# Kernel tuning notes

Hardware: AMD Instinct MI355X
Metric: run time of the kernel (lower is better)

Reference implementation:

```python
import jax, jax.numpy as jnp
import numpy as np

MAX_SCALE_MUL = float(np.log(100.0))
EPS = 1e-12

def _l2norm(t):
    # F.normalize(dim=-1): x / max(||x||_2, eps)
    n = jnp.sqrt(jnp.sum(t * t, axis=-1, keepdims=True))
    return t / jnp.maximum(n, EPS)

def setup_inputs() -> dict:
    key = jax.random.key(0)
    ks = jax.random.split(key, 6)
    B, L, C, H = 2, 2048, 1024, 16
    x = jax.random.normal(ks[0], (B, L, C), dtype=jnp.float32)
    attn_bias = jax.random.normal(ks[1], (1, 1, L, L), dtype=jnp.float32) * 0.02
    W_qkv = jax.random.normal(ks[2], (3 * C, C), dtype=jnp.float32) * (1.0 / np.sqrt(C))
    q_bias = jnp.zeros((C,), dtype=jnp.float32)
    v_bias = jnp.zeros((C,), dtype=jnp.float32)
    scale_mul_1H11 = jnp.full((1, H, 1, 1), np.log(4.0), dtype=jnp.float32)
    W_proj = jax.random.normal(ks[3], (C, C), dtype=jnp.float32) * (1.0 / np.sqrt(C))
    b_proj = jnp.zeros((C,), dtype=jnp.float32)
    return {"x": x, "attn_bias": attn_bias, "W_qkv": W_qkv, "q_bias": q_bias,
            "v_bias": v_bias, "scale_mul_1H11": scale_mul_1H11,
            "W_proj": W_proj, "b_proj": b_proj}

def reference(x, attn_bias, W_qkv, q_bias, v_bias, scale_mul_1H11, W_proj, b_proj):
    B, L, C = x.shape
    H = scale_mul_1H11.shape[1]
    D = C // H
    # qkv projection (no linear bias) + concatenated (q_bias, 0, v_bias)
    bias = jnp.concatenate([q_bias, jnp.zeros_like(q_bias), v_bias])
    pre_qkv = jnp.einsum('blc,oc->blo', x, W_qkv) + bias  # (B,L,3C)
    qkv = pre_qkv.reshape(B, L, 3, H, D).transpose(2, 0, 3, 1, 4)  # (3,B,H,L,D)
    q, k, v = qkv[0], qkv[1], qkv[2]
    # cosine attention: l2-normalize q,k; q scaled by learned per-head scale
    scale_mul = jnp.exp(jnp.minimum(scale_mul_1H11, MAX_SCALE_MUL))
    q = _l2norm(q) * scale_mul
    k = _l2norm(k)
    # slow_attn_original with scale=1 (attn_l2_norm path)
    attn = jnp.einsum('bhld,bhmd->bhlm', q, k) + attn_bias  # (B,H,L,L)
    attn = jax.nn.softmax(attn, axis=-1)
    oup = jnp.einsum('bhlm,bhmd->bhld', attn, v)  # (B,H,L,D)
    oup = oup.transpose(0, 2, 1, 3).reshape(B, L, C)
    return jnp.einsum('blc,oc->blo', oup, W_proj) + b_proj
```

## Files before the change

### kernel.cpp

```cpp
#include <hip/hip_runtime.h>

typedef short bf16x8 __attribute__((ext_vector_type(8)));
typedef unsigned short u16x8 __attribute__((ext_vector_type(8)));
typedef float f32x4 __attribute__((ext_vector_type(4)));
typedef float f32x16 __attribute__((ext_vector_type(16)));
typedef unsigned int u32x2 __attribute__((ext_vector_type(2)));

#define LOG2E 1.44269504088896340736f

__device__ __forceinline__ float bf2f(unsigned short u) {
  union { unsigned int i; float f; } v; v.i = ((unsigned int)u) << 16; return v.f;
}
__device__ __forceinline__ unsigned short f2bf(float f) {
  union { float fl; unsigned int i; } v; v.fl = f;
  unsigned int r = v.i + 0x7FFFu + ((v.i >> 16) & 1u);
  return (unsigned short)(r >> 16);
}
__device__ __forceinline__ unsigned int cvt_pk_bf16(float lo, float hi) {
  unsigned int d;
  asm("v_cvt_pk_bf16_f32 %0, %1, %2" : "=v"(d) : "v"(lo), "v"(hi));
  return d;
}
__device__ __forceinline__ void perm_swap(unsigned int& a, unsigned int& b) {
  asm("v_permlane32_swap_b32 %0, %1" : "+v"(a), "+v"(b));
}
__device__ __forceinline__ bf16x8 mk8(unsigned int a, unsigned int b,
                                      unsigned int c, unsigned int d) {
  union { unsigned int u[4]; bf16x8 v; } r;
  r.u[0] = a; r.u[1] = b; r.u[2] = c; r.u[3] = d;
  return r.v;
}
__device__ __forceinline__ void gload_lds16(const void* g, void* l) {
  __builtin_amdgcn_global_load_lds(
      (const __attribute__((address_space(1))) void*)g,
      (__attribute__((address_space(3))) void*)l, 16, 0, 0);
}

__global__ __launch_bounds__(256) void cvt_all(const float* __restrict__ x,
                                               const float* __restrict__ wqkv,
                                               const float* __restrict__ wproj,
                                               unsigned short* __restrict__ xb,
                                               unsigned short* __restrict__ wqb,
                                               unsigned short* __restrict__ wpb) {
  int i = blockIdx.x * 256 + threadIdx.x;
  const float* src; unsigned short* dst; int off;
  if (i < 524288)       { src = x;     dst = xb;  off = i; }
  else if (i < 917504)  { src = wqkv;  dst = wqb; off = i - 524288; }
  else                  { src = wproj; dst = wpb; off = i - 917504; }
  float4 a = ((const float4*)src)[2 * off];
  float4 b = ((const float4*)src)[2 * off + 1];
  u16x8 o;
  o[0] = f2bf(a.x); o[1] = f2bf(a.y); o[2] = f2bf(a.z); o[3] = f2bf(a.w);
  o[4] = f2bf(b.x); o[5] = f2bf(b.y); o[6] = f2bf(b.z); o[7] = f2bf(b.w);
  ((u16x8*)dst)[off] = o;
}

__global__ __launch_bounds__(256) void prep_bias(const float* __restrict__ bias,
                                                 unsigned short* __restrict__ biasArr) {
  int tid = blockIdx.x * 256 + threadIdx.x;
  int kg = tid & 1;
  int l = (tid >> 1) & 63;
  int w = (tid >> 7) & 3;
  int kb = (tid >> 9) & 31;
  int qt = (tid >> 14) & 15;
  int q = qt * 128 + w * 32 + (l & 31);
  int kbase = kb * 64 + kg * 32 + (l >> 5) * 4;
  const float* src = bias + (size_t)q * 2048 + kbase;
  u16x8 oa, ob;
#pragma unroll
  for (int rr = 0; rr < 4; ++rr) {
    float4 g = *(const float4*)(src + rr * 8);
    unsigned short e0 = f2bf(g.x * LOG2E), e1 = f2bf(g.y * LOG2E);
    unsigned short e2 = f2bf(g.z * LOG2E), e3 = f2bf(g.w * LOG2E);
    if (rr < 2) {
      oa[rr * 4 + 0] = e0; oa[rr * 4 + 1] = e1; oa[rr * 4 + 2] = e2; oa[rr * 4 + 3] = e3;
    } else {
      ob[(rr - 2) * 4 + 0] = e0; ob[(rr - 2) * 4 + 1] = e1;
      ob[(rr - 2) * 4 + 2] = e2; ob[(rr - 2) * 4 + 3] = e3;
    }
  }
  int base = (((qt * 32 + kb) * 4 + w) * 4 + kg * 2) * 64 + l;
  ((u16x8*)biasArr)[base] = oa;
  ((u16x8*)biasArr)[base + 64] = ob;
}

template <bool F32OUT>
__global__ __launch_bounds__(256) void gemm_nt(const unsigned short* __restrict__ A,
                                               const unsigned short* __restrict__ B,
                                               void* __restrict__ Cout,
                                               const float* __restrict__ bias,
                                               int M, int N, int K) {
  __shared__ __align__(16) unsigned short a_lds[128 * 64];
  __shared__ __align__(16) unsigned short b_lds[128 * 64];
  const int t = threadIdx.x;
  const int lane = t & 63, w = t >> 6;
  const int wm = w >> 1, wn = w & 1;
  const int r16 = lane >> 4, c16 = lane & 15;
  const int m0 = blockIdx.y * 128, n0 = blockIdx.x * 128;
  f32x4 acc[4][4] = {};
  for (int k0 = 0; k0 < K; k0 += 64) {
#pragma unroll
    for (int i = 0; i < 4; ++i) {
      int s = i * 256 + t;
      int row = s >> 3, c = s & 7;
      int cs = c ^ (row & 7);
      gload_lds16(A + (size_t)(m0 + row) * K + k0 + cs * 8, (char*)a_lds + s * 16);
      gload_lds16(B + (size_t)(n0 + row) * K + k0 + cs * 8, (char*)b_lds + s * 16);
    }
    __syncthreads();
#pragma unroll
    for (int ks = 0; ks < 2; ++ks) {
      bf16x8 af[4], bfr[4];
#pragma unroll
      for (int mi = 0; mi < 4; ++mi) {
        int row = wm * 64 + mi * 16 + c16;
        int ch = (r16 + ks * 4) ^ (row & 7);
        af[mi] = *(const bf16x8*)&a_lds[row * 64 + ch * 8];
      }
#pragma unroll
      for (int ni = 0; ni < 4; ++ni) {
        int row = wn * 64 + ni * 16 + c16;
        int ch = (r16 + ks * 4) ^ (row & 7);
        bfr[ni] = *(const bf16x8*)&b_lds[row * 64 + ch * 8];
      }
#pragma unroll
      for (int mi = 0; mi < 4; ++mi)
#pragma unroll
        for (int ni = 0; ni < 4; ++ni)
          acc[mi][ni] = __builtin_amdgcn_mfma_f32_16x16x32_bf16(af[mi], bfr[ni], acc[mi][ni], 0, 0, 0);
    }
    __syncthreads();
  }
#pragma unroll
  for (int mi = 0; mi < 4; ++mi)
#pragma unroll
    for (int ni = 0; ni < 4; ++ni)
#pragma unroll
      for (int r = 0; r < 4; ++r) {
        int m = m0 + wm * 64 + mi * 16 + r16 * 4 + r;
        int n = n0 + wn * 64 + ni * 16 + c16;
        float v = acc[mi][ni][r];
        if constexpr (F32OUT) {
          ((float*)Cout)[(size_t)m * N + n] = v + bias[n];
        } else {
          ((unsigned short*)Cout)[(size_t)m * N + n] = f2bf(v);
        }
      }
}

__global__ __launch_bounds__(256) void norm_pack(const unsigned short* __restrict__ pre,
                                                 const float* __restrict__ q_bias,
                                                 const float* __restrict__ v_bias,
                                                 const float* __restrict__ scale_mul,
                                                 unsigned short* __restrict__ qo,
                                                 unsigned short* __restrict__ ko,
                                                 unsigned short* __restrict__ vto) {
  __shared__ float tl[64][65];
  const int t = threadIdx.x;
  const int li = t >> 2, dq = t & 3;
  const int tile = blockIdx.x;
  const int sl = blockIdx.y;
  const int qkv = sl >> 4, h = sl & 15;
  const int b = tile >> 5, lt = tile & 31;
  const int l = lt * 64 + li;
  const int dbase = dq * 16;
  const unsigned short* src = pre + ((size_t)b * 2048 + l) * 3072 + qkv * 1024 + h * 64 + dbase;
  float v[16];
  bf16x8 x0 = *(const bf16x8*)src;
  bf16x8 x1 = *(const bf16x8*)(src + 8);
#pragma unroll
  for (int j = 0; j < 8; ++j) {
    v[j] = bf2f((unsigned short)x0[j]);
    v[8 + j] = bf2f((unsigned short)x1[j]);
  }
  if (qkv == 0) {
#pragma unroll
    for (int j = 0; j < 16; ++j) v[j] += q_bias[h * 64 + dbase + j];
  } else if (qkv == 2) {
#pragma unroll
    for (int j = 0; j < 16; ++j) v[j] += v_bias[h * 64 + dbase + j];
  }
  if (qkv < 2) {
    float ss = 0.f;
#pragma unroll
    for (int j = 0; j < 16; ++j) ss += v[j] * v[j];
    ss += __shfl_xor(ss, 1);
    ss += __shfl_xor(ss, 2);
    float inv = 1.0f / fmaxf(sqrtf(ss), 1e-12f);
    if (qkv == 0) inv *= __expf(fminf(scale_mul[h], 4.6051701859880914f));
    u16x8 o0, o1;
#pragma unroll
    for (int j = 0; j < 8; ++j) {
      o0[j] = f2bf(v[j] * inv);
      o1[j] = f2bf(v[8 + j] * inv);
    }
    unsigned short* dst = (qkv == 0 ? qo : ko) + ((size_t)(b * 16 + h) * 2048 + l) * 64 + dbase;
    *(u16x8*)dst = o0;
    *(u16x8*)(dst + 8) = o1;
  } else {
#pragma unroll
    for (int j = 0; j < 16; ++j) tl[li][dbase + j] = v[j];
    __syncthreads();
    const int d = li;
    const int lb = dq * 16;
    u16x8 o0, o1;
#pragma unroll
    for (int j = 0; j < 8; ++j) {
      o0[j] = f2bf(tl[lb + j][d]);
      o1[j] = f2bf(tl[lb + 8 + j][d]);
    }
    unsigned short* dst = vto + ((size_t)(b * 16 + h) * 64 + d) * 2048 + lt * 64 + lb;
    *(u16x8*)dst = o0;
    *(u16x8*)(dst + 8) = o1;
  }
}

__global__ __launch_bounds__(256) void attn_fwd(const unsigned short* __restrict__ qb,
                                                const unsigned short* __restrict__ kbuf,
                                                const unsigned short* __restrict__ vtb,
                                                const unsigned short* __restrict__ biasArr,
                                                unsigned short* __restrict__ oup) {
  __shared__ __align__(16) unsigned short k_lds[4096];
  __shared__ __align__(16) unsigned short vt_lds[4096];
  __shared__ __align__(16) unsigned short b_lds[8192];
  const int t = threadIdx.x;
  const int lane = t & 63, w = t >> 6;
  const int l31 = lane & 31, hi = lane >> 5;
  const int bid = blockIdx.x;
  const int swz = (bid & 7) * 64 + (bid >> 3);
  const int bh = swz >> 4;
  const int qt = swz & 15;
  const int q0 = qt * 128;
  const int h = bh & 15;
  const size_t base = (size_t)bh * 2048 * 64;
  const unsigned short* kp = kbuf + base + (size_t)(t & 31) * 64 +
                             ((t >> 6) & 3) * 16 + ((t >> 5) & 1) * 8;
  const unsigned short* vp = vtb + base + (size_t)(t & 31) * 2048 +
                             ((t >> 6) & 3) * 16 + ((t >> 5) & 1) * 8;
  const unsigned short* bsrc = biasArr + (size_t)qt * 262144 + t * 8;
  bf16x8 qf[4];
  {
    const unsigned short* qp = qb + base + (size_t)(q0 + w * 32 + l31) * 64 + hi * 8;
    qf[0] = *(const bf16x8*)qp;
    qf[1] = *(const bf16x8*)(qp + 16);
    qf[2] = *(const bf16x8*)(qp + 32);
    qf[3] = *(const bf16x8*)(qp + 48);
  }
  f32x16 o0 = {}, o1 = {};
  float ls0 = 0.f, ls1 = 0.f;
  const unsigned short* bl = b_lds + w * 2048 + lane * 8;

  for (int kb = 0; kb < 32; ++kb) {
    gload_lds16(kp + (size_t)kb * 4096, (char*)k_lds + t * 16);
    gload_lds16(kp + (size_t)kb * 4096 + 2048, (char*)k_lds + t * 16 + 4096);
    gload_lds16(vp + kb * 64, (char*)vt_lds + t * 16);
    gload_lds16(vp + kb * 64 + 32 * 2048, (char*)vt_lds + t * 16 + 4096);
#pragma unroll
    for (int i = 0; i < 4; ++i)
      gload_lds16(bsrc + kb * 8192 + i * 2048, (char*)b_lds + t * 16 + i * 4096);
    __syncthreads();
    f32x16 s0 = {}, s1 = {};
    __builtin_amdgcn_s_setprio(1);
#pragma unroll
    for (int dc = 0; dc < 4; ++dc) {
      bf16x8 kf0 = *(const bf16x8*)&k_lds[dc * 512 + lane * 8];
      bf16x8 kf1 = *(const bf16x8*)&k_lds[(4 + dc) * 512 + lane * 8];
      s0 = __builtin_amdgcn_mfma_f32_32x32x16_bf16(kf0, qf[dc], s0, 0, 0, 0);
      s1 = __builtin_amdgcn_mfma_f32_32x32x16_bf16(kf1, qf[dc], s1, 0, 0, 0);
    }
    __builtin_amdgcn_s_setprio(0);
    bf16x8 b0 = *(const bf16x8*)(bl);
    bf16x8 b1 = *(const bf16x8*)(bl + 512);
    bf16x8 b2 = *(const bf16x8*)(bl + 1024);
    bf16x8 b3 = *(const bf16x8*)(bl + 1536);
    float p0[16], p1[16];
#pragma unroll
    for (int r = 0; r < 8; ++r) {
      p0[r] = __builtin_amdgcn_exp2f(__builtin_fmaf(s0[r], LOG2E, bf2f((unsigned short)b0[r])));
      p0[8 + r] = __builtin_amdgcn_exp2f(__builtin_fmaf(s0[8 + r], LOG2E, bf2f((unsigned short)b1[r])));
      p1[r] = __builtin_amdgcn_exp2f(__builtin_fmaf(s1[r], LOG2E, bf2f((unsigned short)b2[r])));
      p1[8 + r] = __builtin_amdgcn_exp2f(__builtin_fmaf(s1[8 + r], LOG2E, bf2f((unsigned short)b3[r])));
    }
#pragma unroll
    for (int r = 0; r < 16; ++r) { ls0 += p0[r]; ls1 += p1[r]; }
    unsigned int x0 = cvt_pk_bf16(p0[0], p0[1]), x1 = cvt_pk_bf16(p0[2], p0[3]);
    unsigned int y0 = cvt_pk_bf16(p0[4], p0[5]), y1 = cvt_pk_bf16(p0[6], p0[7]);
    unsigned int z0 = cvt_pk_bf16(p0[8], p0[9]), z1 = cvt_pk_bf16(p0[10], p0[11]);
    unsigned int w0 = cvt_pk_bf16(p0[12], p0[13]), w1 = cvt_pk_bf16(p0[14], p0[15]);
    perm_swap(x0, y0); perm_swap(x1, y1); perm_swap(z0, w0); perm_swap(z1, w1);
    bf16x8 pf0 = mk8(x0, x1, y0, y1);
    bf16x8 pf1 = mk8(z0, z1, w0, w1);
    unsigned int a0 = cvt_pk_bf16(p1[0], p1[1]), a1 = cvt_pk_bf16(p1[2], p1[3]);
    unsigned int c0 = cvt_pk_bf16(p1[4], p1[5]), c1 = cvt_pk_bf16(p1[6], p1[7]);
    unsigned int d0 = cvt_pk_bf16(p1[8], p1[9]), d1 = cvt_pk_bf16(p1[10], p1[11]);
    unsigned int e0 = cvt_pk_bf16(p1[12], p1[13]), e1 = cvt_pk_bf16(p1[14], p1[15]);
    perm_swap(a0, c0); perm_swap(a1, c1); perm_swap(d0, e0); perm_swap(d1, e1);
    bf16x8 pf2 = mk8(a0, a1, c0, c1);
    bf16x8 pf3 = mk8(d0, d1, e0, e1);
    bf16x8 pf[4] = {pf0, pf1, pf2, pf3};
    __builtin_amdgcn_s_setprio(1);
#pragma unroll
    for (int kc = 0; kc < 4; ++kc) {
      bf16x8 vf0 = *(const bf16x8*)&vt_lds[kc * 512 + lane * 8];
      bf16x8 vf1 = *(const bf16x8*)&vt_lds[(4 + kc) * 512 + lane * 8];
      o0 = __builtin_amdgcn_mfma_f32_32x32x16_bf16(vf0, pf[kc], o0, 0, 0, 0);
      o1 = __builtin_amdgcn_mfma_f32_32x32x16_bf16(vf1, pf[kc], o1, 0, 0, 0);
    }
    __builtin_amdgcn_s_setprio(0);
    __syncthreads();
  }
  float lsum = ls0 + ls1;
  lsum += __shfl_xor(lsum, 32);
  float inv = 1.0f / lsum;
  const int b = bh >> 4;
  unsigned short* orow = oup + ((size_t)b * 2048 + q0 + w * 32 + l31) * 1024 + h * 64;
#pragma unroll
  for (int dg = 0; dg < 2; ++dg) {
#pragma unroll
    for (int rr = 0; rr < 4; ++rr) {
      float v0 = (dg ? o1[rr * 4 + 0] : o0[rr * 4 + 0]) * inv;
      float v1 = (dg ? o1[rr * 4 + 1] : o0[rr * 4 + 1]) * inv;
      float v2 = (dg ? o1[rr * 4 + 2] : o0[rr * 4 + 2]) * inv;
      float v3 = (dg ? o1[rr * 4 + 3] : o0[rr * 4 + 3]) * inv;
      u32x2 pk2;
      pk2[0] = cvt_pk_bf16(v0, v1);
      pk2[1] = cvt_pk_bf16(v2, v3);
      int d = dg * 32 + rr * 8 + hi * 4;
      *(u32x2*)(orow + d) = pk2;
    }
  }
}

extern "C" void kernel_launch(void* const* d_in, const int* in_sizes, int n_in,
                              void* d_out, int out_size, void* d_ws, size_t ws_size,
                              hipStream_t stream) {
  const float* x = (const float*)d_in[0];
  const float* attn_bias = (const float*)d_in[1];
  const float* W_qkv = (const float*)d_in[2];
  const float* q_bias = (const float*)d_in[3];
  const float* v_bias = (const float*)d_in[4];
  const float* scale_mul = (const float*)d_in[5];
  const float* W_proj = (const float*)d_in[6];
  const float* b_proj = (const float*)d_in[7];
  float* out = (float*)d_out;
  char* ws = (char*)d_ws;

  unsigned short* x_bf = (unsigned short*)(ws + 0);
  unsigned short* wqkv_bf = (unsigned short*)(ws + 8388608);
  unsigned short* wproj_bf = (unsigned short*)(ws + 14680064);
  unsigned short* biasArr = (unsigned short*)(ws + 16777216);
  unsigned short* q_pk = (unsigned short*)(ws + 25165824);
  unsigned short* k_pk = (unsigned short*)(ws + 33554432);
  unsigned short* vt_pk = (unsigned short*)(ws + 41943040);
  unsigned short* oup_bf = (unsigned short*)(ws + 50331648);
  unsigned short* pre_qkv = (unsigned short*)(ws + 58720256);

  cvt_all<<<4096, 256, 0, stream>>>(x, W_qkv, W_proj, x_bf, wqkv_bf, wproj_bf);
  prep_bias<<<1024, 256, 0, stream>>>(attn_bias, biasArr);
  gemm_nt<false><<<dim3(24, 32), 256, 0, stream>>>(x_bf, wqkv_bf, (void*)pre_qkv, nullptr,
                                                   4096, 3072, 1024);
  norm_pack<<<dim3(64, 48), 256, 0, stream>>>(pre_qkv, q_bias, v_bias, scale_mul,
                                              q_pk, k_pk, vt_pk);
  attn_fwd<<<512, 256, 0, stream>>>(q_pk, k_pk, vt_pk, biasArr, oup_bf);
  gemm_nt<true><<<dim3(8, 32), 256, 0, stream>>>(oup_bf, wproj_bf, (void*)out, b_proj,
                                                 4096, 1024, 1024);
}
```

Baseline: 151.7 us.

## Split attention key range across two wave groups per block with LDS reduction

The attention kernel now launches 512 threads per block, and the key loop is split into two halves. Each group of four waves processes 16 key blocks using its own LDS buffers. At the end, the second group writes its partial output accumulators and row sums to LDS, and the first group adds them and writes the normalized result. This doubles the waves in flight to hide memory and exp latency. The cost is a doubled LDS footprint, a cross-group reduction, and block-wide syncs that now couple both halves.

```diff
diff --git a/kernel.cpp b/kernel.cpp
--- a/kernel.cpp
+++ b/kernel.cpp
@@ -215,16 +215,19 @@
   }
 }
 
-__global__ __launch_bounds__(256) void attn_fwd(const unsigned short* __restrict__ qb,
+__global__ __launch_bounds__(512) void attn_fwd(const unsigned short* __restrict__ qb,
                                                 const unsigned short* __restrict__ kbuf,
                                                 const unsigned short* __restrict__ vtb,
                                                 const unsigned short* __restrict__ biasArr,
                                                 unsigned short* __restrict__ oup) {
-  __shared__ __align__(16) unsigned short k_lds[4096];
-  __shared__ __align__(16) unsigned short vt_lds[4096];
-  __shared__ __align__(16) unsigned short b_lds[8192];
+  __shared__ __align__(16) unsigned short k_lds[2][4096];
+  __shared__ __align__(16) unsigned short vt_lds[2][4096];
+  __shared__ __align__(16) unsigned short b_lds[2][8192];
   const int t = threadIdx.x;
   const int lane = t & 63, w = t >> 6;
+  const int sp = w >> 2;
+  const int wq = w & 3;
+  const int tt = t & 255;
   const int l31 = lane & 31, hi = lane >> 5;
   const int bid = blockIdx.x;
   const int swz = (bid & 7) * 64 + (bid >> 3);
@@ -233,14 +236,14 @@
   const int q0 = qt * 128;
   const int h = bh & 15;
   const size_t base = (size_t)bh * 2048 * 64;
-  const unsigned short* kp = kbuf + base + (size_t)(t & 31) * 64 +
-                             ((t >> 6) & 3) * 16 + ((t >> 5) & 1) * 8;
-  const unsigned short* vp = vtb + base + (size_t)(t & 31) * 2048 +
-                             ((t >> 6) & 3) * 16 + ((t >> 5) & 1) * 8;
-  const unsigned short* bsrc = biasArr + (size_t)qt * 262144 + t * 8;
+  const unsigned short* kp = kbuf + base + (size_t)(tt & 31) * 64 +
+                             ((tt >> 6) & 3) * 16 + ((tt >> 5) & 1) * 8;
+  const unsigned short* vp = vtb + base + (size_t)(tt & 31) * 2048 +
+                             ((tt >> 6) & 3) * 16 + ((tt >> 5) & 1) * 8;
+  const unsigned short* bsrc = biasArr + (size_t)qt * 262144 + tt * 8;
   bf16x8 qf[4];
   {
-    const unsigned short* qp = qb + base + (size_t)(q0 + w * 32 + l31) * 64 + hi * 8;
+    const unsigned short* qp = qb + base + (size_t)(q0 + wq * 32 + l31) * 64 + hi * 8;
     qf[0] = *(const bf16x8*)qp;
     qf[1] = *(const bf16x8*)(qp + 16);
     qf[2] = *(const bf16x8*)(qp + 32);
@@ -248,23 +251,24 @@
   }
   f32x16 o0 = {}, o1 = {};
   float ls0 = 0.f, ls1 = 0.f;
-  const unsigned short* bl = b_lds + w * 2048 + lane * 8;
-
-  for (int kb = 0; kb < 32; ++kb) {
-    gload_lds16(kp + (size_t)kb * 4096, (char*)k_lds + t * 16);
-    gload_lds16(kp + (size_t)kb * 4096 + 2048, (char*)k_lds + t * 16 + 4096);
-    gload_lds16(vp + kb * 64, (char*)vt_lds + t * 16);
-    gload_lds16(vp + kb * 64 + 32 * 2048, (char*)vt_lds + t * 16 + 4096);
+  const unsigned short* bl = b_lds[sp] + wq * 2048 + lane * 8;
+
+  for (int kbl = 0; kbl < 16; ++kbl) {
+    const int kb = sp * 16 + kbl;
+    gload_lds16(kp + (size_t)kb * 4096, (char*)k_lds[sp] + tt * 16);
+    gload_lds16(kp + (size_t)kb * 4096 + 2048, (char*)k_lds[sp] + tt * 16 + 4096);
+    gload_lds16(vp + kb * 64, (char*)vt_lds[sp] + tt * 16);
+    gload_lds16(vp + kb * 64 + 32 * 2048, (char*)vt_lds[sp] + tt * 16 + 4096);
 #pragma unroll
     for (int i = 0; i < 4; ++i)
-      gload_lds16(bsrc + kb * 8192 + i * 2048, (char*)b_lds + t * 16 + i * 4096);
+      gload_lds16(bsrc + kb * 8192 + i * 2048, (char*)b_lds[sp] + tt * 16 + i * 4096);
     __syncthreads();
     f32x16 s0 = {}, s1 = {};
     __builtin_amdgcn_s_setprio(1);
 #pragma unroll
     for (int dc = 0; dc < 4; ++dc) {
-      bf16x8 kf0 = *(const bf16x8*)&k_lds[dc * 512 + lane * 8];
-      bf16x8 kf1 = *(const bf16x8*)&k_lds[(4 + dc) * 512 + lane * 8];
+      bf16x8 kf0 = *(const bf16x8*)&k_lds[sp][dc * 512 + lane * 8];
+      bf16x8 kf1 = *(const bf16x8*)&k_lds[sp][(4 + dc) * 512 + lane * 8];
       s0 = __builtin_amdgcn_mfma_f32_32x32x16_bf16(kf0, qf[dc], s0, 0, 0, 0);
       s1 = __builtin_amdgcn_mfma_f32_32x32x16_bf16(kf1, qf[dc], s1, 0, 0, 0);
     }
@@ -301,32 +305,50 @@
     __builtin_amdgcn_s_setprio(1);
 #pragma unroll
     for (int kc = 0; kc < 4; ++kc) {
-      bf16x8 vf0 = *(const bf16x8*)&vt_lds[kc * 512 + lane * 8];
-      bf16x8 vf1 = *(const bf16x8*)&vt_lds[(4 + kc) * 512 + lane * 8];
+      bf16x8 vf0 = *(const bf16x8*)&vt_lds[sp][kc * 512 + lane * 8];
+      bf16x8 vf1 = *(const bf16x8*)&vt_lds[sp][(4 + kc) * 512 + lane * 8];
       o0 = __builtin_amdgcn_mfma_f32_32x32x16_bf16(vf0, pf[kc], o0, 0, 0, 0);
       o1 = __builtin_amdgcn_mfma_f32_32x32x16_bf16(vf1, pf[kc], o1, 0, 0, 0);
     }
     __builtin_amdgcn_s_setprio(0);
     __syncthreads();
   }
-  float lsum = ls0 + ls1;
-  lsum += __shfl_xor(lsum, 32);
-  float inv = 1.0f / lsum;
-  const int b = bh >> 4;
-  unsigned short* orow = oup + ((size_t)b * 2048 + q0 + w * 32 + l31) * 1024 + h * 64;
-#pragma unroll
-  for (int dg = 0; dg < 2; ++dg) {
-#pragma unroll
-    for (int rr = 0; rr < 4; ++rr) {
-      float v0 = (dg ? o1[rr * 4 + 0] : o0[rr * 4 + 0]) * inv;
-      float v1 = (dg ? o1[rr * 4 + 1] : o0[rr * 4 + 1]) * inv;
-      float v2 = (dg ? o1[rr * 4 + 2] : o0[rr * 4 + 2]) * inv;
-      float v3 = (dg ? o1[rr * 4 + 3] : o0[rr * 4 + 3]) * inv;
-      u32x2 pk2;
-      pk2[0] = cvt_pk_bf16(v0, v1);
-      pk2[1] = cvt_pk_bf16(v2, v3);
-      int d = dg * 32 + rr * 8 + hi * 4;
-      *(u32x2*)(orow + d) = pk2;
+  {
+    float* fO = (float*)b_lds;
+    float* fL = (float*)k_lds;
+    const int idx = (wq * 64 + lane) * 32;
+    if (sp == 1) {
+#pragma unroll
+      for (int i = 0; i < 16; ++i) { fO[idx + i] = o0[i]; fO[idx + 16 + i] = o1[i]; }
+      fL[(wq * 64 + lane) * 2] = ls0;
+      fL[(wq * 64 + lane) * 2 + 1] = ls1;
+    }
+    __syncthreads();
+    if (sp == 0) {
+#pragma unroll
+      for (int i = 0; i < 16; ++i) { o0[i] += fO[idx + i]; o1[i] += fO[idx + 16 + i]; }
+      ls0 += fL[(wq * 64 + lane) * 2];
+      ls1 += fL[(wq * 64 + lane) * 2 + 1];
+      float lsum = ls0 + ls1;
+      lsum += __shfl_xor(lsum, 32);
+      float inv = 1.0f / lsum;
+      const int b = bh >> 4;
+      unsigned short* orow = oup + ((size_t)b * 2048 + q0 + wq * 32 + l31) * 1024 + h * 64;
+#pragma unroll
+      for (int dg = 0; dg < 2; ++dg) {
+#pragma unroll
+        for (int rr = 0; rr < 4; ++rr) {
+          float v0 = (dg ? o1[rr * 4 + 0] : o0[rr * 4 + 0]) * inv;
+          float v1 = (dg ? o1[rr * 4 + 1] : o0[rr * 4 + 1]) * inv;
+          float v2 = (dg ? o1[rr * 4 + 2] : o0[rr * 4 + 2]) * inv;
+          float v3 = (dg ? o1[rr * 4 + 3] : o0[rr * 4 + 3]) * inv;
+          u32x2 pk2;
+          pk2[0] = cvt_pk_bf16(v0, v1);
+          pk2[1] = cvt_pk_bf16(v2, v3);
+          int d = dg * 32 + rr * 8 + hi * 4;
+          *(u32x2*)(orow + d) = pk2;
+        }
+      }
     }
   }
 }
@@ -361,7 +383,7 @@
                                                    4096, 3072, 1024);
   norm_pack<<<dim3(64, 48), 256, 0, stream>>>(pre_qkv, q_bias, v_bias, scale_mul,
                                               q_pk, k_pk, vt_pk);
-  attn_fwd<<<512, 256, 0, stream>>>(q_pk, k_pk, vt_pk, biasArr, oup_bf);
+  attn_fwd<<<512, 512, 0, stream>>>(q_pk, k_pk, vt_pk, biasArr, oup_bf);
   gemm_nt<true><<<dim3(8, 32), 256, 0, stream>>>(oup_bf, wproj_bf, (void*)out, b_proj,
                                                  4096, 1024, 1024);
 }
```

After: 173.8 us. 1.15x slower.

## Double-buffer attention K/V/bias tiles and use narrower-tile output projection GEMM

Applied to the files above, without the earlier changes.

The attention kernel now double-buffers its K, V^T and bias LDS tiles. It prefetches the next key block while computing the current one and needs only one barrier per iteration instead of two. This is meant to hide global-to-LDS latency behind the MFMA and exp work, at the cost of twice the LDS (64KB), which may lower occupancy. The output projection also switches to a 128x64 tile GEMM, doubling the block count from 256 to 512 so more CUs are busy on the 4096x1024 output.

```diff
diff --git a/kernel.cpp b/kernel.cpp
--- a/kernel.cpp
+++ b/kernel.cpp
@@ -139,6 +139,76 @@
       for (int r = 0; r < 4; ++r) {
         int m = m0 + wm * 64 + mi * 16 + r16 * 4 + r;
         int n = n0 + wn * 64 + ni * 16 + c16;
+        float v = acc[mi][ni][r];
+        if constexpr (F32OUT) {
+          ((float*)Cout)[(size_t)m * N + n] = v + bias[n];
+        } else {
+          ((unsigned short*)Cout)[(size_t)m * N + n] = f2bf(v);
+        }
+      }
+}
+
+template <bool F32OUT>
+__global__ __launch_bounds__(256) void gemm_nt64(const unsigned short* __restrict__ A,
+                                                 const unsigned short* __restrict__ B,
+                                                 void* __restrict__ Cout,
+                                                 const float* __restrict__ bias,
+                                                 int M, int N, int K) {
+  __shared__ __align__(16) unsigned short a_lds[128 * 64];
+  __shared__ __align__(16) unsigned short b_lds[64 * 64];
+  const int t = threadIdx.x;
+  const int lane = t & 63, w = t >> 6;
+  const int wm = w >> 1, wn = w & 1;
+  const int r16 = lane >> 4, c16 = lane & 15;
+  const int m0 = blockIdx.y * 128, n0 = blockIdx.x * 64;
+  f32x4 acc[4][2] = {};
+  for (int k0 = 0; k0 < K; k0 += 64) {
+#pragma unroll
+    for (int i = 0; i < 4; ++i) {
+      int s = i * 256 + t;
+      int row = s >> 3, c = s & 7;
+      int cs = c ^ (row & 7);
+      gload_lds16(A + (size_t)(m0 + row) * K + k0 + cs * 8, (char*)a_lds + s * 16);
+    }
+#pragma unroll
+    for (int i = 0; i < 2; ++i) {
+      int s = i * 256 + t;
+      int row = s >> 3, c = s & 7;
+      int cs = c ^ (row & 7);
+      gload_lds16(B + (size_t)(n0 + row) * K + k0 + cs * 8, (char*)b_lds + s * 16);
+    }
+    __syncthreads();
+#pragma unroll
+    for (int ks = 0; ks < 2; ++ks) {
+      bf16x8 af[4], bfr[2];
+#pragma unroll
+      for (int mi = 0; mi < 4; ++mi) {
+        int row = wm * 64 + mi * 16 + c16;
+        int ch = (r16 + ks * 4) ^ (row & 7);
+        af[mi] = *(const bf16x8*)&a_lds[row * 64 + ch * 8];
+      }
+#pragma unroll
+      for (int ni = 0; ni < 2; ++ni) {
+        int row = wn * 32 + ni * 16 + c16;
+        int ch = (r16 + ks * 4) ^ (row & 7);
+        bfr[ni] = *(const bf16x8*)&b_lds[row * 64 + ch * 8];
+      }
+#pragma unroll
+      for (int mi = 0; mi < 4; ++mi)
+#pragma unroll
+        for (int ni = 0; ni < 2; ++ni)
+          acc[mi][ni] = __builtin_amdgcn_mfma_f32_16x16x32_bf16(af[mi], bfr[ni], acc[mi][ni], 0, 0, 0);
+    }
+    __syncthreads();
+  }
+#pragma unroll
+  for (int mi = 0; mi < 4; ++mi)
+#pragma unroll
+    for (int ni = 0; ni < 2; ++ni)
+#pragma unroll
+      for (int r = 0; r < 4; ++r) {
+        int m = m0 + wm * 64 + mi * 16 + r16 * 4 + r;
+        int n = n0 + wn * 32 + ni * 16 + c16;
         float v = acc[mi][ni][r];
         if constexpr (F32OUT) {
           ((float*)Cout)[(size_t)m * N + n] = v + bias[n];
@@ -220,9 +290,9 @@
                                                 const unsigned short* __restrict__ vtb,
                                                 const unsigned short* __restrict__ biasArr,
                                                 unsigned short* __restrict__ oup) {
-  __shared__ __align__(16) unsigned short k_lds[4096];
-  __shared__ __align__(16) unsigned short vt_lds[4096];
-  __shared__ __align__(16) unsigned short b_lds[8192];
+  __shared__ __align__(16) unsigned short k_lds[2][4096];
+  __shared__ __align__(16) unsigned short vt_lds[2][4096];
+  __shared__ __align__(16) unsigned short b_lds[2][8192];
   const int t = threadIdx.x;
   const int lane = t & 63, w = t >> 6;
   const int l31 = lane & 31, hi = lane >> 5;
@@ -248,27 +318,39 @@
   }
   f32x16 o0 = {}, o1 = {};
   float ls0 = 0.f, ls1 = 0.f;
-  const unsigned short* bl = b_lds + w * 2048 + lane * 8;
+
+  gload_lds16(kp, (char*)k_lds[0] + t * 16);
+  gload_lds16(kp + 2048, (char*)k_lds[0] + t * 16 + 4096);
+  gload_lds16(vp, (char*)vt_lds[0] + t * 16);
+  gload_lds16(vp + 32 * 2048, (char*)vt_lds[0] + t * 16 + 4096);
+#pragma unroll
+  for (int i = 0; i < 4; ++i)
+    gload_lds16(bsrc + i * 2048, (char*)b_lds[0] + t * 16 + i * 4096);
 
   for (int kb = 0; kb < 32; ++kb) {
-    gload_lds16(kp + (size_t)kb * 4096, (char*)k_lds + t * 16);
-    gload_lds16(kp + (size_t)kb * 4096 + 2048, (char*)k_lds + t * 16 + 4096);
-    gload_lds16(vp + kb * 64, (char*)vt_lds + t * 16);
-    gload_lds16(vp + kb * 64 + 32 * 2048, (char*)vt_lds + t * 16 + 4096);
-#pragma unroll
-    for (int i = 0; i < 4; ++i)
-      gload_lds16(bsrc + kb * 8192 + i * 2048, (char*)b_lds + t * 16 + i * 4096);
-    __syncthreads();
+    const int cur = kb & 1;
+    __syncthreads();
+    if (kb + 1 < 32) {
+      const int nxt = cur ^ 1;
+      gload_lds16(kp + (size_t)(kb + 1) * 4096, (char*)k_lds[nxt] + t * 16);
+      gload_lds16(kp + (size_t)(kb + 1) * 4096 + 2048, (char*)k_lds[nxt] + t * 16 + 4096);
+      gload_lds16(vp + (kb + 1) * 64, (char*)vt_lds[nxt] + t * 16);
+      gload_lds16(vp + (kb + 1) * 64 + 32 * 2048, (char*)vt_lds[nxt] + t * 16 + 4096);
+#pragma unroll
+      for (int i = 0; i < 4; ++i)
+        gload_lds16(bsrc + (kb + 1) * 8192 + i * 2048, (char*)b_lds[nxt] + t * 16 + i * 4096);
+    }
     f32x16 s0 = {}, s1 = {};
     __builtin_amdgcn_s_setprio(1);
 #pragma unroll
     for (int dc = 0; dc < 4; ++dc) {
-      bf16x8 kf0 = *(const bf16x8*)&k_lds[dc * 512 + lane * 8];
-      bf16x8 kf1 = *(const bf16x8*)&k_lds[(4 + dc) * 512 + lane * 8];
+      bf16x8 kf0 = *(const bf16x8*)&k_lds[cur][dc * 512 + lane * 8];
+      bf16x8 kf1 = *(const bf16x8*)&k_lds[cur][(4 + dc) * 512 + lane * 8];
       s0 = __builtin_amdgcn_mfma_f32_32x32x16_bf16(kf0, qf[dc], s0, 0, 0, 0);
       s1 = __builtin_amdgcn_mfma_f32_32x32x16_bf16(kf1, qf[dc], s1, 0, 0, 0);
     }
     __builtin_amdgcn_s_setprio(0);
+    const unsigned short* bl = b_lds[cur] + w * 2048 + lane * 8;
     bf16x8 b0 = *(const bf16x8*)(bl);
     bf16x8 b1 = *(const bf16x8*)(bl + 512);
     bf16x8 b2 = *(const bf16x8*)(bl + 1024);
@@ -301,13 +383,12 @@
     __builtin_amdgcn_s_setprio(1);
 #pragma unroll
     for (int kc = 0; kc < 4; ++kc) {
-      bf16x8 vf0 = *(const bf16x8*)&vt_lds[kc * 512 + lane * 8];
-      bf16x8 vf1 = *(const bf16x8*)&vt_lds[(4 + kc) * 512 + lane * 8];
+      bf16x8 vf0 = *(const bf16x8*)&vt_lds[cur][kc * 512 + lane * 8];
+      bf16x8 vf1 = *(const bf16x8*)&vt_lds[cur][(4 + kc) * 512 + lane * 8];
       o0 = __builtin_amdgcn_mfma_f32_32x32x16_bf16(vf0, pf[kc], o0, 0, 0, 0);
       o1 = __builtin_amdgcn_mfma_f32_32x32x16_bf16(vf1, pf[kc], o1, 0, 0, 0);
     }
     __builtin_amdgcn_s_setprio(0);
-    __syncthreads();
   }
   float lsum = ls0 + ls1;
   lsum += __shfl_xor(lsum, 32);
@@ -362,6 +443,6 @@
   norm_pack<<<dim3(64, 48), 256, 0, stream>>>(pre_qkv, q_bias, v_bias, scale_mul,
                                               q_pk, k_pk, vt_pk);
   attn_fwd<<<512, 256, 0, stream>>>(q_pk, k_pk, vt_pk, biasArr, oup_bf);
-  gemm_nt<true><<<dim3(8, 32), 256, 0, stream>>>(oup_bf, wproj_bf, (void*)out, b_proj,
-                                                 4096, 1024, 1024);
-}
+  gemm_nt64<true><<<dim3(16, 32), 256, 0, stream>>>(oup_bf, wproj_bf, (void*)out, b_proj,
+                                                    4096, 1024, 1024);
+}
```

New measurement: 152.5 us. About the same (+0.5%).
